# Performance work log

Hardware: AMD Instinct MI355X
Metric: run time of the kernel (lower is better)

## Reference

```python
import jax, jax.numpy as jnp
import numpy as np

T, N, F_IN = 5, 10000, 16
E = 160000
C = 32          # gat_hidden_dim (per head)
H0 = 2          # heads in layer 0 (concat) -> out 64
GRU = 64
OUT_H = 32


def setup_inputs() -> dict:
    key = jax.random.key(0)
    ks = jax.random.split(key, 24)
    s = 0.1
    inp = {
        "x_seq": jax.random.normal(ks[0], (T, N, F_IN), jnp.float32),
        "edge_index": jax.random.randint(ks[1], (2, E), 0, N, jnp.int32),
        # GAT layer 0: in 16 -> 2 heads x 32, concat -> 64
        "gat0_W": s * jax.random.normal(ks[2], (F_IN, H0 * C), jnp.float32),
        "gat0_asrc": s * jax.random.normal(ks[3], (H0, C), jnp.float32),
        "gat0_adst": s * jax.random.normal(ks[4], (H0, C), jnp.float32),
        "gat0_b": s * jax.random.normal(ks[5], (H0 * C,), jnp.float32),
        "res0_W": s * jax.random.normal(ks[6], (F_IN, H0 * C), jnp.float32),   # [in,out]
        # GAT layer 1: in 64 -> 1 head x 32, no concat -> 32
        "gat1_W": s * jax.random.normal(ks[7], (H0 * C, C), jnp.float32),
        "gat1_asrc": s * jax.random.normal(ks[8], (1, C), jnp.float32),
        "gat1_adst": s * jax.random.normal(ks[9], (1, C), jnp.float32),
        "gat1_b": s * jax.random.normal(ks[10], (C,), jnp.float32),
        "res1_W": s * jax.random.normal(ks[11], (H0 * C, C), jnp.float32),
        # GRU cells (torch GRUCell layout: W_i [3H,in], W_h [3H,H])
        "gru0_Wi": s * jax.random.normal(ks[12], (3 * GRU, C), jnp.float32),
        "gru0_Wh": s * jax.random.normal(ks[13], (3 * GRU, GRU), jnp.float32),
        "gru0_bi": s * jax.random.normal(ks[14], (3 * GRU,), jnp.float32),
        "gru0_bh": s * jax.random.normal(ks[15], (3 * GRU,), jnp.float32),
        "gru1_Wi": s * jax.random.normal(ks[16], (3 * GRU, GRU), jnp.float32),
        "gru1_Wh": s * jax.random.normal(ks[17], (3 * GRU, GRU), jnp.float32),
        "gru1_bi": s * jax.random.normal(ks[18], (3 * GRU,), jnp.float32),
        "gru1_bh": s * jax.random.normal(ks[19], (3 * GRU,), jnp.float32),
        # MLP head
        "fc1_W": s * jax.random.normal(ks[20], (GRU, OUT_H), jnp.float32),
        "fc1_b": s * jax.random.normal(ks[21], (OUT_H,), jnp.float32),
        "fc2_W": s * jax.random.normal(ks[22], (OUT_H, 1), jnp.float32),
        "fc2_b": s * jax.random.normal(ks[23], (1,), jnp.float32),
    }
    return inp


def _gat(x, src, dst, n, W, a_src, a_dst, b, heads, concat):
    ch = W.shape[1] // heads
    xw = (x @ W).reshape(n, heads, ch)                      # [N,H,C]
    al_s = (xw * a_src).sum(-1)                             # [N,H]
    al_d = (xw * a_dst).sum(-1)
    e = jax.nn.leaky_relu(al_s[src] + al_d[dst], 0.2)       # [Etot,H]
    m = jax.ops.segment_max(e, dst, num_segments=n)
    ex = jnp.exp(e - m[dst])
    den = jax.ops.segment_sum(ex, dst, num_segments=n)
    alpha = ex / (den[dst] + 1e-16)                         # scatter-softmax
    out = jax.ops.segment_sum(alpha[:, :, None] * xw[src], dst, num_segments=n)
    out = out.reshape(n, heads * ch) if concat else out.mean(axis=1)
    return out + b


def _gru(x, h, Wi, Wh, bi, bh):
    gi = x @ Wi.T + bi
    gh = h @ Wh.T + bh
    i_r, i_z, i_n = jnp.split(gi, 3, axis=-1)
    h_r, h_z, h_n = jnp.split(gh, 3, axis=-1)
    r = jax.nn.sigmoid(i_r + h_r)
    z = jax.nn.sigmoid(i_z + h_z)
    nn_ = jnp.tanh(i_n + r * h_n)
    return (1.0 - z) * nn_ + z * h


def reference(x_seq, edge_index,
              gat0_W, gat0_asrc, gat0_adst, gat0_b, res0_W,
              gat1_W, gat1_asrc, gat1_adst, gat1_b, res1_W,
              gru0_Wi, gru0_Wh, gru0_bi, gru0_bh,
              gru1_Wi, gru1_Wh, gru1_bi, gru1_bh,
              fc1_W, fc1_b, fc2_W, fc2_b):
    n = x_seq.shape[1]
    loops = jnp.arange(n, dtype=edge_index.dtype)
    src = jnp.concatenate([edge_index[0], loops])           # PyG adds self-loops
    dst = jnp.concatenate([edge_index[1], loops])

    def step(carry, x_t):
        h0, h1 = carry
        x1 = jax.nn.elu(_gat(x_t, src, dst, n, gat0_W, gat0_asrc, gat0_adst, gat0_b, 2, True)) + x_t @ res0_W
        x2 = jax.nn.elu(_gat(x1, src, dst, n, gat1_W, gat1_asrc, gat1_adst, gat1_b, 1, False)) + x1 @ res1_W
        h0 = _gru(x2, h0, gru0_Wi, gru0_Wh, gru0_bi, gru0_bh)
        h1 = _gru(h0, h1, gru1_Wi, gru1_Wh, gru1_bi, gru1_bh)
        return (h0, h1), None

    h0 = jnp.zeros((n, gru0_Wh.shape[1]), x_seq.dtype)
    h1 = jnp.zeros((n, gru1_Wh.shape[1]), x_seq.dtype)
    (h0, h1), _ = jax.lax.scan(step, (h0, h1), x_seq)
    h = jax.nn.relu(h1 @ fc1_W + fc1_b)
    return h @ fc2_W + fc2_b                                # [N,1]
```

## Files before the change

### kernel.cpp

```cpp
#include <hip/hip_runtime.h>
#include <hip/hip_bf16.h>
#include <math.h>

#define T_STEPS 5
#define NNODES  10000
#define NM      (T_STEPS * NNODES)
#define F_IN    16
#define NEDGES  160000
#define ETOT    (NEDGES + NNODES)
#define GW      8
#define GNPW    5

#define RL(v, k)  __int_as_float(__builtin_amdgcn_readlane(__float_as_int(v), (k)))
#define RLI(v, k) __builtin_amdgcn_readlane((v), (k))

__global__ __launch_bounds__(256) void k_count(const int* __restrict__ ei, int* __restrict__ counts) {
    int idx = blockIdx.x * 256 + threadIdx.x;
    if (idx >= ETOT) return;
    int dst = (idx < NEDGES) ? ei[NEDGES + idx] : (idx - NEDGES);
    atomicAdd(&counts[dst], 1);
}

__global__ __launch_bounds__(1024) void k_scan(const int* __restrict__ counts, int* __restrict__ offs) {
    __shared__ int ssum[1024];
    int t = threadIdx.x;
    const int chunk = (NNODES + 1023) / 1024;
    int start = t * chunk, end = min(start + chunk, NNODES);
    int s = 0;
    for (int i = start; i < end; i++) s += counts[i];
    ssum[t] = s;
    __syncthreads();
    for (int off = 1; off < 1024; off <<= 1) {
        int v = (t >= off) ? ssum[t - off] : 0;
        __syncthreads();
        ssum[t] += v;
        __syncthreads();
    }
    int excl = (t == 0) ? 0 : ssum[t - 1];
    for (int i = start; i < end; i++) { offs[i] = excl; excl += counts[i]; }
    if (t == 1023) offs[NNODES] = ssum[1023];
}

__global__ __launch_bounds__(256) void k_fill(const int* __restrict__ ei, const int* __restrict__ offs,
                                              int* __restrict__ cursor, int* __restrict__ csr) {
    int idx = blockIdx.x * 256 + threadIdx.x;
    if (idx >= ETOT) return;
    int src, dst;
    if (idx < NEDGES) { src = ei[idx]; dst = ei[NEDGES + idx]; }
    else              { src = dst = idx - NEDGES; }
    int p = atomicAdd(&cursor[dst], 1);
    csr[offs[dst] + p] = src;
}

__global__ __launch_bounds__(256) void k_transpose(const float* __restrict__ Wi0, const float* __restrict__ Wh0,
                                                   const float* __restrict__ Wi1, const float* __restrict__ Wh1,
                                                   float* __restrict__ WiT0, float* __restrict__ WhT0,
                                                   float* __restrict__ WiT1, float* __restrict__ WhT1,
                                                   float2* __restrict__ h0rz, float* __restrict__ h0n,
                                                   float2* __restrict__ i1rz, float* __restrict__ i1n,
                                                   float2* __restrict__ h1rz, float* __restrict__ h1n) {
    int idx = blockIdx.x * 256 + threadIdx.x;
    if (idx < 6144)  { int k = idx / 192, r = idx % 192; WiT0[idx] = Wi0[r * 32 + k]; return; }
    idx -= 6144;
    if (idx < 12288) { int k = idx / 192, r = idx % 192; WhT0[idx] = Wh0[r * 64 + k]; return; }
    idx -= 12288;
    if (idx < 12288) { int k = idx / 192, r = idx % 192; WiT1[idx] = Wi1[r * 64 + k]; return; }
    idx -= 12288;
    if (idx < 12288) { int k = idx / 192, r = idx % 192; WhT1[idx] = Wh1[r * 64 + k]; return; }
    idx -= 12288;
    if (idx < 4096) { int k = idx >> 6, c = idx & 63;
                      h0rz[idx] = make_float2(Wh0[c * 64 + k], Wh0[(64 + c) * 64 + k]);
                      h0n[idx]  = Wh0[(128 + c) * 64 + k]; return; }
    idx -= 4096;
    if (idx < 4096) { int k = idx >> 6, c = idx & 63;
                      i1rz[idx] = make_float2(Wi1[c * 64 + k], Wi1[(64 + c) * 64 + k]);
                      i1n[idx]  = Wi1[(128 + c) * 64 + k]; return; }
    idx -= 4096;
    if (idx < 4096) { int k = idx >> 6, c = idx & 63;
                      h1rz[idx] = make_float2(Wh1[c * 64 + k], Wh1[(64 + c) * 64 + k]);
                      h1n[idx]  = Wh1[(128 + c) * 64 + k]; }
}

__global__ __launch_bounds__(256) void k_mm0_all(const float* __restrict__ x,
                                                 const float* __restrict__ W,
                                                 const float* __restrict__ Wres,
                                                 const float* __restrict__ asrc,
                                                 const float* __restrict__ adst,
                                                 float* __restrict__ xw, float* __restrict__ xres,
                                                 float* __restrict__ als, float* __restrict__ ald) {
    int wave = threadIdx.x >> 6, lane = threadIdx.x & 63;
    int m = blockIdx.x * 4 + wave;
    if (m >= NM) return;
    const float* xr = x + (size_t)m * F_IN;
    float xreg[F_IN];
#pragma unroll
    for (int k = 0; k < F_IN; k++) xreg[k] = xr[k];
    float acc = 0.f, accr = 0.f;
#pragma unroll
    for (int k = 0; k < F_IN; k++) {
        acc  += xreg[k] * W[k * 64 + lane];
        accr += xreg[k] * Wres[k * 64 + lane];
    }
    xw[(size_t)m * 64 + lane]   = acc;
    xres[(size_t)m * 64 + lane] = accr;
    float ps = acc * asrc[lane], pd = acc * adst[lane];
    for (int off = 16; off; off >>= 1) {
        ps += __shfl_down(ps, off, 32);
        pd += __shfl_down(pd, off, 32);
    }
    if ((lane & 31) == 0) {
        int h = lane >> 5;
        als[m * 2 + h] = ps;
        ald[m * 2 + h] = pd;
    }
}

__global__ __launch_bounds__(256) void k_gat0_all(const float* __restrict__ xw,
                                                  const float* __restrict__ xres,
                                                  const float* __restrict__ als,
                                                  const float* __restrict__ ald,
                                                  const int* __restrict__ offs, const int* __restrict__ csr,
                                                  const float* __restrict__ b,
                                                  const float* __restrict__ W1,
                                                  const float* __restrict__ Wres1,
                                                  const float* __restrict__ as1,
                                                  const float* __restrict__ ad1v,
                                                  float* __restrict__ xw1, float* __restrict__ xres1,
                                                  float* __restrict__ als1, float* __restrict__ ald1) {
    int wave = threadIdx.x >> 6, lane = threadIdx.x & 63;
    int m = blockIdx.x * 4 + wave;
    if (m >= NM) return;
    int t = m / NNODES;
    int node = m - t * NNODES;
    int base = t * NNODES;
    int beg = offs[node], end = offs[node + 1];
    int deg = end - beg;
    float ad0 = ald[m * 2 + 0], ad1 = ald[m * 2 + 1];
    float acc;
    if (deg <= 64) {
        int s = 0; float e0 = -INFINITY, e1 = -INFINITY;
        if (lane < deg) {
            s = base + csr[beg + lane];
            e0 = als[s * 2 + 0] + ad0; e0 = e0 > 0.f ? e0 : 0.2f * e0;
            e1 = als[s * 2 + 1] + ad1; e1 = e1 > 0.f ? e1 : 0.2f * e1;
        }
        float m0 = e0, m1 = e1;
        for (int o = 32; o; o >>= 1) {
            m0 = fmaxf(m0, __shfl_xor(m0, o));
            m1 = fmaxf(m1, __shfl_xor(m1, o));
        }
        float ex0 = (lane < deg) ? __expf(e0 - m0) : 0.f;
        float ex1 = (lane < deg) ? __expf(e1 - m1) : 0.f;
        float d0 = ex0, d1 = ex1;
        for (int o = 32; o; o >>= 1) {
            d0 += __shfl_xor(d0, o);
            d1 += __shfl_xor(d1, o);
        }
        ex0 *= 1.f / (d0 + 1e-16f);
        ex1 *= 1.f / (d1 + 1e-16f);
        float a0 = 0.f, a1 = 0.f, a2 = 0.f, a3 = 0.f;
        int i = 0;
        for (; i + 4 <= deg; i += 4) {
            int   s0 = RLI(s, i),     s1 = RLI(s, i + 1), s2 = RLI(s, i + 2), s3 = RLI(s, i + 3);
            float u0 = RL(ex0, i),    v0 = RL(ex1, i);
            float u1 = RL(ex0, i+1),  v1 = RL(ex1, i+1);
            float u2 = RL(ex0, i+2),  v2 = RL(ex1, i+2);
            float u3 = RL(ex0, i+3),  v3 = RL(ex1, i+3);
            a0 += (lane < 32 ? u0 : v0) * xw[(size_t)s0 * 64 + lane];
            a1 += (lane < 32 ? u1 : v1) * xw[(size_t)s1 * 64 + lane];
            a2 += (lane < 32 ? u2 : v2) * xw[(size_t)s2 * 64 + lane];
            a3 += (lane < 32 ? u3 : v3) * xw[(size_t)s3 * 64 + lane];
        }
        for (; i < deg; i++) {
            int s0 = RLI(s, i);
            float u = RL(ex0, i), v = RL(ex1, i);
            a0 += (lane < 32 ? u : v) * xw[(size_t)s0 * 64 + lane];
        }
        acc = (a0 + a1) + (a2 + a3);
    } else {
        float m0 = -INFINITY, m1 = -INFINITY;
        for (int i = beg + lane; i < end; i += 64) {
            int s = base + csr[i];
            float e0 = als[s * 2 + 0] + ad0; e0 = e0 > 0.f ? e0 : 0.2f * e0;
            float e1 = als[s * 2 + 1] + ad1; e1 = e1 > 0.f ? e1 : 0.2f * e1;
            m0 = fmaxf(m0, e0); m1 = fmaxf(m1, e1);
        }
        for (int o = 32; o; o >>= 1) {
            m0 = fmaxf(m0, __shfl_xor(m0, o));
            m1 = fmaxf(m1, __shfl_xor(m1, o));
        }
        float d0 = 0.f, d1 = 0.f;
        for (int i = beg + lane; i < end; i += 64) {
            int s = base + csr[i];
            float e0 = als[s * 2 + 0] + ad0; e0 = e0 > 0.f ? e0 : 0.2f * e0;
            float e1 = als[s * 2 + 1] + ad1; e1 = e1 > 0.f ? e1 : 0.2f * e1;
            d0 += __expf(e0 - m0); d1 += __expf(e1 - m1);
        }
        for (int o = 32; o; o >>= 1) { d0 += __shfl_xor(d0, o); d1 += __shfl_xor(d1, o); }
        float inv0 = 1.f / (d0 + 1e-16f), inv1 = 1.f / (d1 + 1e-16f);
        acc = 0.f;
        for (int i = beg; i < end; i++) {
            int s = base + csr[i];
            float e, wgt;
            if (lane < 32) { e = als[s * 2 + 0] + ad0; e = e > 0.f ? e : 0.2f * e; wgt = __expf(e - m0) * inv0; }
            else           { e = als[s * 2 + 1] + ad1; e = e > 0.f ? e : 0.2f * e; wgt = __expf(e - m1) * inv1; }
            acc += wgt * xw[(size_t)s * 64 + lane];
        }
    }
    float x1v = acc + b[lane];
    x1v = x1v > 0.f ? x1v : expm1f(x1v);
    x1v += xres[(size_t)m * 64 + lane];
    int j = lane & 31;
    const float* Wp = (lane < 32) ? W1 : Wres1;
    float pacc = 0.f;
#pragma unroll
    for (int k = 0; k < 64; k++) {
        float xv = RL(x1v, k);
        pacc += xv * Wp[k * 32 + j];
    }
    if (lane < 32) xw1[(size_t)m * 32 + j]   = pacc;
    else           xres1[(size_t)m * 32 + j] = pacc;
    float ps = (lane < 32) ? pacc * as1[j]  : 0.f;
    float pd = (lane < 32) ? pacc * ad1v[j] : 0.f;
    for (int o = 16; o; o >>= 1) {
        ps += __shfl_down(ps, o, 32);
        pd += __shfl_down(pd, o, 32);
    }
    if (lane == 0) { als1[m] = ps; ald1[m] = pd; }
}

__global__ __launch_bounds__(256) void k_gat1_all(const float* __restrict__ xw1,
                                                  const float* __restrict__ xres1,
                                                  const float* __restrict__ als1,
                                                  const float* __restrict__ ald1,
                                                  const int* __restrict__ offs, const int* __restrict__ csr,
                                                  const float* __restrict__ b,
                                                  const float* __restrict__ WiT0,
                                                  const float* __restrict__ bi0,
                                                  float* __restrict__ gi0) {
    int wave = threadIdx.x >> 6, lane = threadIdx.x & 63;
    int m = blockIdx.x * 4 + wave;
    if (m >= NM) return;
    int t = m / NNODES;
    int node = m - t * NNODES;
    int base = t * NNODES;
    int beg = offs[node], end = offs[node + 1];
    int deg = end - beg;
    float adv = ald1[m];
    int ch = lane & 31, half = lane >> 5;
    float aggr;
    if (deg <= 64) {
        int s = 0; float e = -INFINITY;
        if (lane < deg) {
            s = base + csr[beg + lane];
            e = als1[s] + adv; e = e > 0.f ? e : 0.2f * e;
        }
        float mx = e;
        for (int o = 32; o; o >>= 1) mx = fmaxf(mx, __shfl_xor(mx, o));
        float ex = (lane < deg) ? __expf(e - mx) : 0.f;
        float d = ex;
        for (int o = 32; o; o >>= 1) d += __shfl_xor(d, o);
        ex *= 1.f / (d + 1e-16f);
        float acc = 0.f;
        for (int i = 0; i < deg; i += 2) {
            int i2 = (i + 1 < deg) ? i + 1 : i;
            int   sa = RLI(s, i),  sb = RLI(s, i2);
            float wa = RL(ex, i),  wb = RL(ex, i2);
            if (i + 1 >= deg) wb = 0.f;
            int   sm = half ? sb : sa;
            float wm = half ? wb : wa;
            acc += wm * xw1[(size_t)sm * 32 + ch];
        }
        acc += __shfl_xor(acc, 32);
        aggr = acc;
    } else {
        float mx = -INFINITY;
        for (int i = beg + lane; i < end; i += 64) {
            float e = als1[base + csr[i]] + adv; e = e > 0.f ? e : 0.2f * e;
            mx = fmaxf(mx, e);
        }
        for (int o = 32; o; o >>= 1) mx = fmaxf(mx, __shfl_xor(mx, o));
        float d = 0.f;
        for (int i = beg + lane; i < end; i += 64) {
            float e = als1[base + csr[i]] + adv; e = e > 0.f ? e : 0.2f * e;
            d += __expf(e - mx);
        }
        for (int o = 32; o; o >>= 1) d += __shfl_xor(d, o);
        float inv = 1.f / (d + 1e-16f);
        float acc = 0.f;
        for (int i = beg; i < end; i++) {
            int s = base + csr[i];
            float e = als1[s] + adv; e = e > 0.f ? e : 0.2f * e;
            float wgt = __expf(e - mx) * inv;
            acc += wgt * xw1[(size_t)s * 32 + ch];
        }
        aggr = acc;
    }
    float v = aggr + b[ch];
    v = v > 0.f ? v : expm1f(v);
    float x2v = v + xres1[(size_t)m * 32 + ch];
#pragma unroll
    for (int p = 0; p < 3; p++) {
        float accp = bi0[p * 64 + lane];
#pragma unroll 8
        for (int k = 0; k < 32; k++) {
            accp += RL(x2v, k) * WiT0[k * 192 + p * 64 + lane];
        }
        gi0[(size_t)m * 192 + p * 64 + lane] = accp;
    }
}

__global__ __launch_bounds__(512) void k_gruhead_p(const float* __restrict__ gi0,
                                                   const float4* __restrict__ wblob,
                                                   const float* __restrict__ bh0,
                                                   const float* __restrict__ bi1, const float* __restrict__ bh1,
                                                   const float* __restrict__ fc1W, const float* __restrict__ fc1b,
                                                   const float* __restrict__ fc2W, const float* __restrict__ fc2b,
                                                   float* __restrict__ out) {
    extern __shared__ char ldsraw[];
    float2* Lh0rz = (float2*)ldsraw;
    float*  Lh0n  = (float*)(ldsraw + 32768);
    float2* Li1rz = (float2*)(ldsraw + 49152);
    float*  Li1n  = (float*)(ldsraw + 81920);
    float2* Lh1rz = (float2*)(ldsraw + 98304);
    float*  Lh1n  = (float*)(ldsraw + 131072);
    int tid = threadIdx.x, wave = tid >> 6, lane = tid & 63;
    int node0 = (blockIdx.x * GW + wave) * GNPW;

    {
        float4* D = (float4*)ldsraw;
#pragma unroll
        for (int i = 0; i < 18; i++) D[tid + i * 512] = wblob[tid + i * 512];
    }
    __syncthreads();

    float bhr0 = bh0[lane], bhz0 = bh0[64 + lane], bhn0 = bh0[128 + lane];
    float bir1 = bi1[lane] + bh1[lane];
    float biz1 = bi1[64 + lane] + bh1[64 + lane];
    float bin1 = bi1[128 + lane], bhn1 = bh1[128 + lane];

    float h0[GNPW] = {0.f, 0.f, 0.f, 0.f, 0.f};
    float h1[GNPW] = {0.f, 0.f, 0.f, 0.f, 0.f};

    for (int t = 0; t < T_STEPS; t++) {
        float gr[GNPW], gz[GNPW], gin[GNPW], ghn[GNPW];
        size_t gb = ((size_t)t * NNODES + node0) * 192;
#pragma unroll
        for (int n = 0; n < GNPW; n++) {
            gr[n]  = gi0[gb + n * 192 + lane] + bhr0;
            gz[n]  = gi0[gb + n * 192 + 64 + lane] + bhz0;
            gin[n] = gi0[gb + n * 192 + 128 + lane];
            ghn[n] = bhn0;
        }
#pragma unroll 4
        for (int k = 0; k < 64; k++) {
            float2 wrz = Lh0rz[k * 64 + lane];
            float  wn  = Lh0n[k * 64 + lane];
#pragma unroll
            for (int n = 0; n < GNPW; n++) {
                float hv = RL(h0[n], k);
                gr[n] += hv * wrz.x; gz[n] += hv * wrz.y; ghn[n] += hv * wn;
            }
        }
#pragma unroll
        for (int n = 0; n < GNPW; n++) {
            float r = 1.f / (1.f + __expf(-gr[n]));
            float z = 1.f / (1.f + __expf(-gz[n]));
            float nn = tanhf(gin[n] + r * ghn[n]);
            h0[n] = (1.f - z) * nn + z * h0[n];
        }

#pragma unroll
        for (int n = 0; n < GNPW; n++) { gr[n] = bir1; gz[n] = biz1; gin[n] = bin1; }
#pragma unroll 4
        for (int k = 0; k < 64; k++) {
            float2 wrz = Li1rz[k * 64 + lane];
            float  wn  = Li1n[k * 64 + lane];
#pragma unroll
            for (int n = 0; n < GNPW; n++) {
                float xv = RL(h0[n], k);
                gr[n] += xv * wrz.x; gz[n] += xv * wrz.y; gin[n] += xv * wn;
            }
        }
#pragma unroll
        for (int n = 0; n < GNPW; n++) ghn[n] = bhn1;
#pragma unroll 4
        for (int k = 0; k < 64; k++) {
            float2 wrz = Lh1rz[k * 64 + lane];
            float  wn  = Lh1n[k * 64 + lane];
#pragma unroll
            for (int n = 0; n < GNPW; n++) {
                float hv = RL(h1[n], k);
                gr[n] += hv * wrz.x; gz[n] += hv * wrz.y; ghn[n] += hv * wn;
            }
        }
#pragma unroll
        for (int n = 0; n < GNPW; n++) {
            float r = 1.f / (1.f + __expf(-gr[n]));
            float z = 1.f / (1.f + __expf(-gz[n]));
            float nn = tanhf(gin[n] + r * ghn[n]);
            h1[n] = (1.f - z) * nn + z * h1[n];
        }
    }

    int j = lane & 31, half = lane >> 5;
#pragma unroll
    for (int p = 0; p < 3; p++) {
        int ne = 2 * p;
        int no = (2 * p + 1 < GNPW) ? 2 * p + 1 : 2 * p;
        float a = fc1b[j];
#pragma unroll
        for (int k = 0; k < 64; k++) {
            float he = RL(h1[ne], k);
            float ho = RL(h1[no], k);
            a += (half ? ho : he) * fc1W[k * 32 + j];
        }
        a = fmaxf(a, 0.f);
        float v = a * fc2W[j];
        for (int o = 16; o; o >>= 1) v += __shfl_down(v, o, 32);
        if ((lane & 31) == 0 && 2 * p + half < GNPW) out[node0 + 2 * p + half] = v + fc2b[0];
    }
}

__global__ __launch_bounds__(512) void k_gruhead(const float* __restrict__ gi0,
                                                 const float* __restrict__ WhT0,
                                                 const float* __restrict__ WiT1,
                                                 const float* __restrict__ WhT1,
                                                 const float* __restrict__ bh0,
                                                 const float* __restrict__ bi1, const float* __restrict__ bh1,
                                                 const float* __restrict__ fc1W, const float* __restrict__ fc1b,
                                                 const float* __restrict__ fc2W, const float* __restrict__ fc2b,
                                                 float* __restrict__ out) {
    __shared__ float lw[64 * 192];
    int tid = threadIdx.x;
    int wave = tid >> 6, lane = tid & 63;
    int node0 = (blockIdx.x * GW + wave) * GNPW;

    float bhr0 = bh0[lane], bhz0 = bh0[64 + lane], bhn0 = bh0[128 + lane];
    float bir1 = bi1[lane] + bh1[lane];
    float biz1 = bi1[64 + lane] + bh1[64 + lane];
    float bin1 = bi1[128 + lane], bhn1 = bh1[128 + lane];

    float h0[GNPW] = {0.f, 0.f, 0.f, 0.f, 0.f};
    float h1[GNPW] = {0.f, 0.f, 0.f, 0.f, 0.f};

    auto stage = [&](const float* __restrict__ src) {
        __syncthreads();
        const float4* s4 = (const float4*)src;
        float4* d4 = (float4*)lw;
#pragma unroll
        for (int i = 0; i < 6; i++) d4[tid + i * 512] = s4[tid + i * 512];
        __syncthreads();
    };

    for (int t = 0; t < T_STEPS; t++) {
        float gr[GNPW], gz[GNPW], gin[GNPW], ghn[GNPW];
        size_t gb = ((size_t)t * NNODES + node0) * 192;
#pragma unroll
        for (int n = 0; n < GNPW; n++) {
            gr[n]  = gi0[gb + n * 192 + lane] + bhr0;
            gz[n]  = gi0[gb + n * 192 + 64 + lane] + bhz0;
            gin[n] = gi0[gb + n * 192 + 128 + lane];
            ghn[n] = bhn0;
        }
        stage(WhT0);
#pragma unroll 4
        for (int k = 0; k < 64; k++) {
            float wr = lw[k * 192 + lane];
            float wz = lw[k * 192 + 64 + lane];
            float wn = lw[k * 192 + 128 + lane];
#pragma unroll
            for (int n = 0; n < GNPW; n++) {
                float hv = RL(h0[n], k);
                gr[n] += hv * wr; gz[n] += hv * wz; ghn[n] += hv * wn;
            }
        }
#pragma unroll
        for (int n = 0; n < GNPW; n++) {
            float r = 1.f / (1.f + __expf(-gr[n]));
            float z = 1.f / (1.f + __expf(-gz[n]));
            float nn = tanhf(gin[n] + r * ghn[n]);
            h0[n] = (1.f - z) * nn + z * h0[n];
        }
#pragma unroll
        for (int n = 0; n < GNPW; n++) { gr[n] = bir1; gz[n] = biz1; gin[n] = bin1; }
        stage(WiT1);
#pragma unroll 4
        for (int k = 0; k < 64; k++) {
            float wir = lw[k * 192 + lane];
            float wiz = lw[k * 192 + 64 + lane];
            float win = lw[k * 192 + 128 + lane];
#pragma unroll
            for (int n = 0; n < GNPW; n++) {
                float xv = RL(h0[n], k);
                gr[n] += xv * wir; gz[n] += xv * wiz; gin[n] += xv * win;
            }
        }
#pragma unroll
        for (int n = 0; n < GNPW; n++) ghn[n] = bhn1;
        stage(WhT1);
#pragma unroll 4
        for (int k = 0; k < 64; k++) {
            float whr = lw[k * 192 + lane];
            float whz = lw[k * 192 + 64 + lane];
            float whn = lw[k * 192 + 128 + lane];
#pragma unroll
            for (int n = 0; n < GNPW; n++) {
                float hv = RL(h1[n], k);
                gr[n] += hv * whr; gz[n] += hv * whz; ghn[n] += hv * whn;
            }
        }
#pragma unroll
        for (int n = 0; n < GNPW; n++) {
            float r = 1.f / (1.f + __expf(-gr[n]));
            float z = 1.f / (1.f + __expf(-gz[n]));
            float nn = tanhf(gin[n] + r * ghn[n]);
            h1[n] = (1.f - z) * nn + z * h1[n];
        }
    }

    int j = lane & 31, half = lane >> 5;
#pragma unroll
    for (int p = 0; p < 3; p++) {
        int ne = 2 * p;
        int no = (2 * p + 1 < GNPW) ? 2 * p + 1 : 2 * p;
        float a = fc1b[j];
#pragma unroll
        for (int k = 0; k < 64; k++) {
            float he = RL(h1[ne], k);
            float ho = RL(h1[no], k);
            a += (half ? ho : he) * fc1W[k * 32 + j];
        }
        a = fmaxf(a, 0.f);
        float v = a * fc2W[j];
        for (int o = 16; o; o >>= 1) v += __shfl_down(v, o, 32);
        if ((lane & 31) == 0 && 2 * p + half < GNPW) out[node0 + 2 * p + half] = v + fc2b[0];
    }
}

extern "C" void kernel_launch(void* const* d_in, const int* in_sizes, int n_in,
                              void* d_out, int out_size, void* d_ws, size_t ws_size,
                              hipStream_t stream) {
    const float* x_seq   = (const float*)d_in[0];
    const int*   ei      = (const int*)d_in[1];
    const float* gat0_W  = (const float*)d_in[2];
    const float* gat0_as = (const float*)d_in[3];
    const float* gat0_ad = (const float*)d_in[4];
    const float* gat0_b  = (const float*)d_in[5];
    const float* res0_W  = (const float*)d_in[6];
    const float* gat1_W  = (const float*)d_in[7];
    const float* gat1_as = (const float*)d_in[8];
    const float* gat1_ad = (const float*)d_in[9];
    const float* gat1_b  = (const float*)d_in[10];
    const float* res1_W  = (const float*)d_in[11];
    const float* gru0_Wi = (const float*)d_in[12];
    const float* gru0_Wh = (const float*)d_in[13];
    const float* gru0_bi = (const float*)d_in[14];
    const float* gru0_bh = (const float*)d_in[15];
    const float* gru1_Wi = (const float*)d_in[16];
    const float* gru1_Wh = (const float*)d_in[17];
    const float* gru1_bi = (const float*)d_in[18];
    const float* gru1_bh = (const float*)d_in[19];
    const float* fc1_W   = (const float*)d_in[20];
    const float* fc1_b   = (const float*)d_in[21];
    const float* fc2_W   = (const float*)d_in[22];
    const float* fc2_b   = (const float*)d_in[23];
    float* out = (float*)d_out;

    char* w = (char*)d_ws;
    size_t off = 0;
    auto take = [&](size_t bytes) { size_t r = off; off += (bytes + 255) & ~(size_t)255; return r; };
    const size_t N = NNODES, M = NM;
    int*   counts = (int*)(w + take(N * 4));
    int*   cursor = (int*)(w + take(N * 4));
    size_t zero_span = off;
    int*   offs   = (int*)(w + take((N + 1) * 4));
    int*   csr    = (int*)(w + take((size_t)ETOT * 4));
    float* xw0    = (float*)(w + take(M * 64 * 4));
    float* xres0  = (float*)(w + take(M * 64 * 4));
    float* als0   = (float*)(w + take(M * 2 * 4));
    float* ald0   = (float*)(w + take(M * 2 * 4));
    float* xw1    = (float*)(w + take(M * 32 * 4));
    float* xres1  = (float*)(w + take(M * 32 * 4));
    float* als1   = (float*)(w + take(M * 4));
    float* ald1   = (float*)(w + take(M * 4));
    float* gi0    = (float*)(w + take(M * 192 * 4));
    float* wiT0   = (float*)(w + take(32 * 192 * 4));
    float* whT0   = (float*)(w + take(64 * 192 * 4));
    float* wiT1   = (float*)(w + take(64 * 192 * 4));
    float* whT1   = (float*)(w + take(64 * 192 * 4));
    char*   blob  = w + take(147456);
    float2* h0rz  = (float2*)blob;
    float*  h0n   = (float*)(blob + 32768);
    float2* i1rz  = (float2*)(blob + 49152);
    float*  i1n   = (float*)(blob + 81920);
    float2* h1rz  = (float2*)(blob + 98304);
    float*  h1n   = (float*)(blob + 131072);

    hipMemsetAsync(w, 0, zero_span, stream);
    const int egrid = (ETOT + 255) / 256;
    k_count<<<egrid, 256, 0, stream>>>(ei, counts);
    k_scan<<<1, 1024, 0, stream>>>(counts, offs);
    k_fill<<<egrid, 256, 0, stream>>>(ei, offs, cursor, csr);
    const int ttot = 6144 + 3 * 12288 + 3 * 4096;
    k_transpose<<<(ttot + 255) / 256, 256, 0, stream>>>(gru0_Wi, gru0_Wh, gru1_Wi, gru1_Wh,
                                                        wiT0, whT0, wiT1, whT1,
                                                        h0rz, h0n, i1rz, i1n, h1rz, h1n);

    const int mgrid = (NM + 3) / 4;
    k_mm0_all<<<mgrid, 256, 0, stream>>>(x_seq, gat0_W, res0_W, gat0_as, gat0_ad, xw0, xres0, als0, ald0);
    k_gat0_all<<<mgrid, 256, 0, stream>>>(xw0, xres0, als0, ald0, offs, csr, gat0_b,
                                          gat1_W, res1_W, gat1_as, gat1_ad,
                                          xw1, xres1, als1, ald1);
    k_gat1_all<<<mgrid, 256, 0, stream>>>(xw1, xres1, als1, ald1, offs, csr, gat1_b,
                                          wiT0, gru0_bi, gi0);

    const int ggrid = NNODES / (GW * GNPW);
    hipError_t ae = hipFuncSetAttribute(reinterpret_cast<const void*>(k_gruhead_p),
                                        hipFuncAttributeMaxDynamicSharedMemorySize, 147456);
    if (ae == hipSuccess) {
        k_gruhead_p<<<ggrid, 512, 147456, stream>>>(gi0, (const float4*)blob,
                                                    gru0_bh, gru1_bi, gru1_bh,
                                                    fc1_W, fc1_b, fc2_W, fc2_b, out);
    } else {
        k_gruhead<<<ggrid, 512, 0, stream>>>(gi0, whT0, wiT1, whT1,
                                             gru0_bh, gru1_bi, gru1_bh,
                                             fc1_W, fc1_b, fc2_W, fc2_b, out);
    }
}
```

Before: 378.6 us.

## Stage GRU hidden states in LDS and fuse second-layer GRU matvecs

```diff
diff --git a/kernel.cpp b/kernel.cpp
--- a/kernel.cpp
+++ b/kernel.cpp
@@ -312,6 +312,7 @@
 
 __global__ __launch_bounds__(512) void k_gruhead_p(const float* __restrict__ gi0,
                                                    const float4* __restrict__ wblob,
+                                                   const float* __restrict__ h1nG,
                                                    const float* __restrict__ bh0,
                                                    const float* __restrict__ bi1, const float* __restrict__ bh1,
                                                    const float* __restrict__ fc1W, const float* __restrict__ fc1b,
@@ -323,15 +324,18 @@
     float2* Li1rz = (float2*)(ldsraw + 49152);
     float*  Li1n  = (float*)(ldsraw + 81920);
     float2* Lh1rz = (float2*)(ldsraw + 98304);
-    float*  Lh1n  = (float*)(ldsraw + 131072);
+    float*  Lh0v  = (float*)(ldsraw + 131072);
+    float*  Lh1v  = (float*)(ldsraw + 141312);
     int tid = threadIdx.x, wave = tid >> 6, lane = tid & 63;
-    int node0 = (blockIdx.x * GW + wave) * GNPW;
+    int nb0 = wave * GNPW;
+    int node0 = blockIdx.x * GW * GNPW + nb0;
 
     {
         float4* D = (float4*)ldsraw;
 #pragma unroll
-        for (int i = 0; i < 18; i++) D[tid + i * 512] = wblob[tid + i * 512];
-    }
+        for (int i = 0; i < 16; i++) D[tid + i * 512] = wblob[tid + i * 512];
+    }
+    for (int i = tid; i < GW * GNPW * 64; i += 512) { Lh0v[i] = 0.f; Lh1v[i] = 0.f; }
     __syncthreads();
 
     float bhr0 = bh0[lane], bhz0 = bh0[64 + lane], bhn0 = bh0[128 + lane];
@@ -339,8 +343,8 @@
     float biz1 = bi1[64 + lane] + bh1[64 + lane];
     float bin1 = bi1[128 + lane], bhn1 = bh1[128 + lane];
 
-    float h0[GNPW] = {0.f, 0.f, 0.f, 0.f, 0.f};
-    float h1[GNPW] = {0.f, 0.f, 0.f, 0.f, 0.f};
+    float h0reg[GNPW] = {0.f, 0.f, 0.f, 0.f, 0.f};
+    float h1reg[GNPW] = {0.f, 0.f, 0.f, 0.f, 0.f};
 
     for (int t = 0; t < T_STEPS; t++) {
         float gr[GNPW], gz[GNPW], gin[GNPW], ghn[GNPW];
@@ -358,7 +362,7 @@
             float  wn  = Lh0n[k * 64 + lane];
 #pragma unroll
             for (int n = 0; n < GNPW; n++) {
-                float hv = RL(h0[n], k);
+                float hv = Lh0v[(nb0 + n) * 64 + k];
                 gr[n] += hv * wrz.x; gz[n] += hv * wrz.y; ghn[n] += hv * wn;
             }
         }
@@ -367,31 +371,26 @@
             float r = 1.f / (1.f + __expf(-gr[n]));
             float z = 1.f / (1.f + __expf(-gz[n]));
             float nn = tanhf(gin[n] + r * ghn[n]);
-            h0[n] = (1.f - z) * nn + z * h0[n];
-        }
-
-#pragma unroll
-        for (int n = 0; n < GNPW; n++) { gr[n] = bir1; gz[n] = biz1; gin[n] = bin1; }
+            h0reg[n] = (1.f - z) * nn + z * h0reg[n];
+            Lh0v[(nb0 + n) * 64 + lane] = h0reg[n];
+        }
+
+#pragma unroll
+        for (int n = 0; n < GNPW; n++) { gr[n] = bir1; gz[n] = biz1; gin[n] = bin1; ghn[n] = bhn1; }
 #pragma unroll 4
         for (int k = 0; k < 64; k++) {
-            float2 wrz = Li1rz[k * 64 + lane];
-            float  wn  = Li1n[k * 64 + lane];
+            float2 wirz = Li1rz[k * 64 + lane];
+            float  win  = Li1n[k * 64 + lane];
+            float2 whrz = Lh1rz[k * 64 + lane];
+            float  whn  = h1nG[k * 64 + lane];
 #pragma unroll
             for (int n = 0; n < GNPW; n++) {
-                float xv = RL(h0[n], k);
-                gr[n] += xv * wrz.x; gz[n] += xv * wrz.y; gin[n] += xv * wn;
-            }
-        }
-#pragma unroll
-        for (int n = 0; n < GNPW; n++) ghn[n] = bhn1;
-#pragma unroll 4
-        for (int k = 0; k < 64; k++) {
-            float2 wrz = Lh1rz[k * 64 + lane];
-            float  wn  = Lh1n[k * 64 + lane];
-#pragma unroll
-            for (int n = 0; n < GNPW; n++) {
-                float hv = RL(h1[n], k);
-                gr[n] += hv * wrz.x; gz[n] += hv * wrz.y; ghn[n] += hv * wn;
+                float xv = Lh0v[(nb0 + n) * 64 + k];
+                float hv = Lh1v[(nb0 + n) * 64 + k];
+                gr[n]  += xv * wirz.x + hv * whrz.x;
+                gz[n]  += xv * wirz.y + hv * whrz.y;
+                gin[n] += xv * win;
+                ghn[n] += hv * whn;
             }
         }
 #pragma unroll
@@ -399,7 +398,8 @@
             float r = 1.f / (1.f + __expf(-gr[n]));
             float z = 1.f / (1.f + __expf(-gz[n]));
             float nn = tanhf(gin[n] + r * ghn[n]);
-            h1[n] = (1.f - z) * nn + z * h1[n];
+            h1reg[n] = (1.f - z) * nn + z * h1reg[n];
+            Lh1v[(nb0 + n) * 64 + lane] = h1reg[n];
         }
     }
 
@@ -411,8 +411,8 @@
         float a = fc1b[j];
 #pragma unroll
         for (int k = 0; k < 64; k++) {
-            float he = RL(h1[ne], k);
-            float ho = RL(h1[no], k);
+            float he = RL(h1reg[ne], k);
+            float ho = RL(h1reg[no], k);
             a += (half ? ho : he) * fc1W[k * 32 + j];
         }
         a = fmaxf(a, 0.f);
@@ -589,13 +589,13 @@
     float* whT0   = (float*)(w + take(64 * 192 * 4));
     float* wiT1   = (float*)(w + take(64 * 192 * 4));
     float* whT1   = (float*)(w + take(64 * 192 * 4));
-    char*   blob  = w + take(147456);
+    char*   blob  = w + take(131072);
     float2* h0rz  = (float2*)blob;
     float*  h0n   = (float*)(blob + 32768);
     float2* i1rz  = (float2*)(blob + 49152);
     float*  i1n   = (float*)(blob + 81920);
     float2* h1rz  = (float2*)(blob + 98304);
-    float*  h1n   = (float*)(blob + 131072);
+    float*  h1n   = (float*)(w + take(4096 * 4));
 
     hipMemsetAsync(w, 0, zero_span, stream);
     const int egrid = (ETOT + 255) / 256;
@@ -617,9 +617,9 @@
 
     const int ggrid = NNODES / (GW * GNPW);
     hipError_t ae = hipFuncSetAttribute(reinterpret_cast<const void*>(k_gruhead_p),
-                                        hipFuncAttributeMaxDynamicSharedMemorySize, 147456);
+                                        hipFuncAttributeMaxDynamicSharedMemorySize, 151552);
     if (ae == hipSuccess) {
-        k_gruhead_p<<<ggrid, 512, 147456, stream>>>(gi0, (const float4*)blob,
+        k_gruhead_p<<<ggrid, 512, 151552, stream>>>(gi0, (const float4*)blob, h1n,
                                                     gru0_bh, gru1_bi, gru1_bh,
                                                     fc1_W, fc1_b, fc2_W, fc2_b, out);
     } else {
```

Result: slower. 395.0 us (+4.3%).

## Merge edge count, weight transpose and layer-0 matmul into one preamble launch

Applied to the files above, without the earlier changes.

```diff
diff --git a/kernel.cpp b/kernel.cpp
--- a/kernel.cpp
+++ b/kernel.cpp
@@ -11,15 +11,12 @@
 #define GW      8
 #define GNPW    5
 
+#define CNT_BLKS 665
+#define TRN_BLKS 216
+#define MM0_BLKS 12500
+
 #define RL(v, k)  __int_as_float(__builtin_amdgcn_readlane(__float_as_int(v), (k)))
 #define RLI(v, k) __builtin_amdgcn_readlane((v), (k))
-
-__global__ __launch_bounds__(256) void k_count(const int* __restrict__ ei, int* __restrict__ counts) {
-    int idx = blockIdx.x * 256 + threadIdx.x;
-    if (idx >= ETOT) return;
-    int dst = (idx < NEDGES) ? ei[NEDGES + idx] : (idx - NEDGES);
-    atomicAdd(&counts[dst], 1);
-}
 
 __global__ __launch_bounds__(1024) void k_scan(const int* __restrict__ counts, int* __restrict__ offs) {
     __shared__ int ssum[1024];
@@ -52,44 +49,53 @@
     csr[offs[dst] + p] = src;
 }
 
-__global__ __launch_bounds__(256) void k_transpose(const float* __restrict__ Wi0, const float* __restrict__ Wh0,
-                                                   const float* __restrict__ Wi1, const float* __restrict__ Wh1,
-                                                   float* __restrict__ WiT0, float* __restrict__ WhT0,
-                                                   float* __restrict__ WiT1, float* __restrict__ WhT1,
-                                                   float2* __restrict__ h0rz, float* __restrict__ h0n,
-                                                   float2* __restrict__ i1rz, float* __restrict__ i1n,
-                                                   float2* __restrict__ h1rz, float* __restrict__ h1n) {
-    int idx = blockIdx.x * 256 + threadIdx.x;
-    if (idx < 6144)  { int k = idx / 192, r = idx % 192; WiT0[idx] = Wi0[r * 32 + k]; return; }
-    idx -= 6144;
-    if (idx < 12288) { int k = idx / 192, r = idx % 192; WhT0[idx] = Wh0[r * 64 + k]; return; }
-    idx -= 12288;
-    if (idx < 12288) { int k = idx / 192, r = idx % 192; WiT1[idx] = Wi1[r * 64 + k]; return; }
-    idx -= 12288;
-    if (idx < 12288) { int k = idx / 192, r = idx % 192; WhT1[idx] = Wh1[r * 64 + k]; return; }
-    idx -= 12288;
-    if (idx < 4096) { int k = idx >> 6, c = idx & 63;
-                      h0rz[idx] = make_float2(Wh0[c * 64 + k], Wh0[(64 + c) * 64 + k]);
-                      h0n[idx]  = Wh0[(128 + c) * 64 + k]; return; }
-    idx -= 4096;
-    if (idx < 4096) { int k = idx >> 6, c = idx & 63;
-                      i1rz[idx] = make_float2(Wi1[c * 64 + k], Wi1[(64 + c) * 64 + k]);
-                      i1n[idx]  = Wi1[(128 + c) * 64 + k]; return; }
-    idx -= 4096;
-    if (idx < 4096) { int k = idx >> 6, c = idx & 63;
-                      h1rz[idx] = make_float2(Wh1[c * 64 + k], Wh1[(64 + c) * 64 + k]);
-                      h1n[idx]  = Wh1[(128 + c) * 64 + k]; }
-}
-
-__global__ __launch_bounds__(256) void k_mm0_all(const float* __restrict__ x,
-                                                 const float* __restrict__ W,
-                                                 const float* __restrict__ Wres,
-                                                 const float* __restrict__ asrc,
-                                                 const float* __restrict__ adst,
-                                                 float* __restrict__ xw, float* __restrict__ xres,
-                                                 float* __restrict__ als, float* __restrict__ ald) {
+__global__ __launch_bounds__(256) void k_preamble(const int* __restrict__ ei, int* __restrict__ counts,
+                                                  const float* __restrict__ Wi0, const float* __restrict__ Wh0,
+                                                  const float* __restrict__ Wi1, const float* __restrict__ Wh1,
+                                                  float* __restrict__ WiT0, float* __restrict__ WhT0,
+                                                  float* __restrict__ WiT1, float* __restrict__ WhT1,
+                                                  float2* __restrict__ h0rz, float* __restrict__ h0n,
+                                                  float2* __restrict__ i1rz, float* __restrict__ i1n,
+                                                  float2* __restrict__ h1rz, float* __restrict__ h1n,
+                                                  const float* __restrict__ x,
+                                                  const float* __restrict__ W,
+                                                  const float* __restrict__ Wres,
+                                                  const float* __restrict__ asrc, const float* __restrict__ adst,
+                                                  float* __restrict__ xw, float* __restrict__ xres,
+                                                  float* __restrict__ als, float* __restrict__ ald) {
+    int b = blockIdx.x;
+    if (b < CNT_BLKS) {
+        int idx = b * 256 + threadIdx.x;
+        if (idx >= ETOT) return;
+        int dst = (idx < NEDGES) ? ei[NEDGES + idx] : (idx - NEDGES);
+        atomicAdd(&counts[dst], 1);
+        return;
+    }
+    if (b < CNT_BLKS + TRN_BLKS) {
+        int idx = (b - CNT_BLKS) * 256 + threadIdx.x;
+        if (idx < 6144)  { int k = idx / 192, r = idx % 192; WiT0[idx] = Wi0[r * 32 + k]; return; }
+        idx -= 6144;
+        if (idx < 12288) { int k = idx / 192, r = idx % 192; WhT0[idx] = Wh0[r * 64 + k]; return; }
+        idx -= 12288;
+        if (idx < 12288) { int k = idx / 192, r = idx % 192; WiT1[idx] = Wi1[r * 64 + k]; return; }
+        idx -= 12288;
+        if (idx < 12288) { int k = idx / 192, r = idx % 192; WhT1[idx] = Wh1[r * 64 + k]; return; }
+        idx -= 12288;
+        if (idx < 4096) { int k = idx >> 6, c = idx & 63;
+                          h0rz[idx] = make_float2(Wh0[c * 64 + k], Wh0[(64 + c) * 64 + k]);
+                          h0n[idx]  = Wh0[(128 + c) * 64 + k]; return; }
+        idx -= 4096;
+        if (idx < 4096) { int k = idx >> 6, c = idx & 63;
+                          i1rz[idx] = make_float2(Wi1[c * 64 + k], Wi1[(64 + c) * 64 + k]);
+                          i1n[idx]  = Wi1[(128 + c) * 64 + k]; return; }
+        idx -= 4096;
+        if (idx < 4096) { int k = idx >> 6, c = idx & 63;
+                          h1rz[idx] = make_float2(Wh1[c * 64 + k], Wh1[(64 + c) * 64 + k]);
+                          h1n[idx]  = Wh1[(128 + c) * 64 + k]; }
+        return;
+    }
     int wave = threadIdx.x >> 6, lane = threadIdx.x & 63;
-    int m = blockIdx.x * 4 + wave;
+    int m = (b - CNT_BLKS - TRN_BLKS) * 4 + wave;
     if (m >= NM) return;
     const float* xr = x + (size_t)m * F_IN;
     float xreg[F_IN];
@@ -160,21 +166,34 @@
         ex1 *= 1.f / (d1 + 1e-16f);
         float a0 = 0.f, a1 = 0.f, a2 = 0.f, a3 = 0.f;
         int i = 0;
-        for (; i + 4 <= deg; i += 4) {
-            int   s0 = RLI(s, i),     s1 = RLI(s, i + 1), s2 = RLI(s, i + 2), s3 = RLI(s, i + 3);
-            float u0 = RL(ex0, i),    v0 = RL(ex1, i);
-            float u1 = RL(ex0, i+1),  v1 = RL(ex1, i+1);
-            float u2 = RL(ex0, i+2),  v2 = RL(ex1, i+2);
-            float u3 = RL(ex0, i+3),  v3 = RL(ex1, i+3);
-            a0 += (lane < 32 ? u0 : v0) * xw[(size_t)s0 * 64 + lane];
-            a1 += (lane < 32 ? u1 : v1) * xw[(size_t)s1 * 64 + lane];
-            a2 += (lane < 32 ? u2 : v2) * xw[(size_t)s2 * 64 + lane];
-            a3 += (lane < 32 ? u3 : v3) * xw[(size_t)s3 * 64 + lane];
+        for (; i + 8 <= deg; i += 8) {
+            int   s0 = RLI(s, i),    s1 = RLI(s, i+1), s2 = RLI(s, i+2), s3 = RLI(s, i+3);
+            int   s4 = RLI(s, i+4),  s5 = RLI(s, i+5), s6 = RLI(s, i+6), s7 = RLI(s, i+7);
+            float x0 = xw[(size_t)s0 * 64 + lane];
+            float x1 = xw[(size_t)s1 * 64 + lane];
+            float x2 = xw[(size_t)s2 * 64 + lane];
+            float x3 = xw[(size_t)s3 * 64 + lane];
+            float x4 = xw[(size_t)s4 * 64 + lane];
+            float x5 = xw[(size_t)s5 * 64 + lane];
+            float x6 = xw[(size_t)s6 * 64 + lane];
+            float x7 = xw[(size_t)s7 * 64 + lane];
+            float u0 = (lane < 32) ? RL(ex0, i)   : RL(ex1, i);
+            float u1 = (lane < 32) ? RL(ex0, i+1) : RL(ex1, i+1);
+            float u2 = (lane < 32) ? RL(ex0, i+2) : RL(ex1, i+2);
+            float u3 = (lane < 32) ? RL(ex0, i+3) : RL(ex1, i+3);
+            float u4 = (lane < 32) ? RL(ex0, i+4) : RL(ex1, i+4);
+            float u5 = (lane < 32) ? RL(ex0, i+5) : RL(ex1, i+5);
+            float u6 = (lane < 32) ? RL(ex0, i+6) : RL(ex1, i+6);
+            float u7 = (lane < 32) ? RL(ex0, i+7) : RL(ex1, i+7);
+            a0 += u0 * x0 + u4 * x4;
+            a1 += u1 * x1 + u5 * x5;
+            a2 += u2 * x2 + u6 * x6;
+            a3 += u3 * x3 + u7 * x7;
         }
         for (; i < deg; i++) {
             int s0 = RLI(s, i);
-            float u = RL(ex0, i), v = RL(ex1, i);
-            a0 += (lane < 32 ? u : v) * xw[(size_t)s0 * 64 + lane];
+            float u = (lane < 32) ? RL(ex0, i) : RL(ex1, i);
+            a0 += u * xw[(size_t)s0 * 64 + lane];
         }
         acc = (a0 + a1) + (a2 + a3);
     } else {
@@ -261,16 +280,38 @@
         float d = ex;
         for (int o = 32; o; o >>= 1) d += __shfl_xor(d, o);
         ex *= 1.f / (d + 1e-16f);
-        float acc = 0.f;
-        for (int i = 0; i < deg; i += 2) {
+        float acc0 = 0.f, acc1 = 0.f;
+        int i = 0;
+        for (; i + 8 <= deg; i += 8) {
+            int   e0 = RLI(s, i),   o0 = RLI(s, i+1);
+            int   e1 = RLI(s, i+2), o1 = RLI(s, i+3);
+            int   e2 = RLI(s, i+4), o2 = RLI(s, i+5);
+            int   e3 = RLI(s, i+6), o3 = RLI(s, i+7);
+            int   sa0 = half ? o0 : e0, sa1 = half ? o1 : e1;
+            int   sa2 = half ? o2 : e2, sa3 = half ? o3 : e3;
+            float xa0 = xw1[(size_t)sa0 * 32 + ch];
+            float xa1 = xw1[(size_t)sa1 * 32 + ch];
+            float xa2 = xw1[(size_t)sa2 * 32 + ch];
+            float xa3 = xw1[(size_t)sa3 * 32 + ch];
+            float we0 = RL(ex, i),   wo0 = RL(ex, i+1);
+            float we1 = RL(ex, i+2), wo1 = RL(ex, i+3);
+            float we2 = RL(ex, i+4), wo2 = RL(ex, i+5);
+            float we3 = RL(ex, i+6), wo3 = RL(ex, i+7);
+            float wa0 = half ? wo0 : we0, wa1 = half ? wo1 : we1;
+            float wa2 = half ? wo2 : we2, wa3 = half ? wo3 : we3;
+            acc0 += wa0 * xa0 + wa2 * xa2;
+            acc1 += wa1 * xa1 + wa3 * xa3;
+        }
+        for (; i < deg; i += 2) {
             int i2 = (i + 1 < deg) ? i + 1 : i;
             int   sa = RLI(s, i),  sb = RLI(s, i2);
             float wa = RL(ex, i),  wb = RL(ex, i2);
             if (i + 1 >= deg) wb = 0.f;
             int   sm = half ? sb : sa;
             float wm = half ? wb : wa;
-            acc += wm * xw1[(size_t)sm * 32 + ch];
-        }
+            acc0 += wm * xw1[(size_t)sm * 32 + ch];
+        }
+        float acc = acc0 + acc1;
         acc += __shfl_xor(acc, 32);
         aggr = acc;
     } else {
@@ -598,22 +639,22 @@
     float*  h1n   = (float*)(blob + 131072);
 
     hipMemsetAsync(w, 0, zero_span, stream);
-    const int egrid = (ETOT + 255) / 256;
-    k_count<<<egrid, 256, 0, stream>>>(ei, counts);
+
+    k_preamble<<<CNT_BLKS + TRN_BLKS + MM0_BLKS, 256, 0, stream>>>(
+        ei, counts,
+        gru0_Wi, gru0_Wh, gru1_Wi, gru1_Wh,
+        wiT0, whT0, wiT1, whT1,
+        h0rz, h0n, i1rz, i1n, h1rz, h1n,
+        x_seq, gat0_W, res0_W, gat0_as, gat0_ad, xw0, xres0, als0, ald0);
+
     k_scan<<<1, 1024, 0, stream>>>(counts, offs);
-    k_fill<<<egrid, 256, 0, stream>>>(ei, offs, cursor, csr);
-    const int ttot = 6144 + 3 * 12288 + 3 * 4096;
-    k_transpose<<<(ttot + 255) / 256, 256, 0, stream>>>(gru0_Wi, gru0_Wh, gru1_Wi, gru1_Wh,
-                                                        wiT0, whT0, wiT1, whT1,
-                                                        h0rz, h0n, i1rz, i1n, h1rz, h1n);
-
-    const int mgrid = (NM + 3) / 4;
-    k_mm0_all<<<mgrid, 256, 0, stream>>>(x_seq, gat0_W, res0_W, gat0_as, gat0_ad, xw0, xres0, als0, ald0);
-    k_gat0_all<<<mgrid, 256, 0, stream>>>(xw0, xres0, als0, ald0, offs, csr, gat0_b,
-                                          gat1_W, res1_W, gat1_as, gat1_ad,
-                                          xw1, xres1, als1, ald1);
-    k_gat1_all<<<mgrid, 256, 0, stream>>>(xw1, xres1, als1, ald1, offs, csr, gat1_b,
-                                          wiT0, gru0_bi, gi0);
+    k_fill<<<CNT_BLKS, 256, 0, stream>>>(ei, offs, cursor, csr);
+
+    k_gat0_all<<<MM0_BLKS, 256, 0, stream>>>(xw0, xres0, als0, ald0, offs, csr, gat0_b,
+                                             gat1_W, res1_W, gat1_as, gat1_ad,
+                                             xw1, xres1, als1, ald1);
+    k_gat1_all<<<MM0_BLKS, 256, 0, stream>>>(xw1, xres1, als1, ald1, offs, csr, gat1_b,
+                                             wiT0, gru0_bi, gi0);
 
     const int ggrid = NNODES / (GW * GNPW);
     hipError_t ae = hipFuncSetAttribute(reinterpret_cast<const void*>(k_gruhead_p),
```

After: 368.0 us. -2.8%, faster.
